# Kernel tuning notes

Hardware: AMD Instinct MI355X
Metric: run time of the kernel (lower is better)

Reference implementation:

```python
import jax, jax.numpy as jnp
import numpy as np

B, N, D, H = 16, 64, 512, 8
DK = D // H


def mish(x):
    return x * jnp.tanh(jax.nn.softplus(x))


def setup_inputs() -> dict:
    key = jax.random.key(0)
    ks = jax.random.split(key, 16)
    s = 1.0 / np.sqrt(D)
    inp = {
        "query_node": jax.random.normal(ks[0], (B, N, D), jnp.float32),
        "value_node": jax.random.normal(ks[1], (B, N, D), jnp.float32),
        "key_edge": jax.random.normal(ks[2], (B, N, N, D), jnp.float32),
        "adj_matrix": jax.random.uniform(ks[3], (B, N, N), jnp.float32),
        "Wq": jax.random.normal(ks[4], (D, D), jnp.float32) * s,
        "bq": jnp.zeros((D,), jnp.float32),
        "Wk": jax.random.normal(ks[5], (D, D), jnp.float32) * s,
        "bk": jnp.zeros((D,), jnp.float32),
        "Wv": jax.random.normal(ks[6], (D, D), jnp.float32) * s,
        "bv": jnp.zeros((D,), jnp.float32),
        "Wn": jax.random.normal(ks[7], (D, D), jnp.float32) * s,
        "bn": jnp.zeros((D,), jnp.float32),
        "We": jax.random.normal(ks[8], (D, D), jnp.float32) * s,
        "be": jnp.zeros((D,), jnp.float32),
    }
    return inp


def reference(query_node, value_node, key_edge, adj_matrix,
              Wq, bq, Wk, bk, Wv, bv, Wn, bn, We, be):
    # distance kernel (computed as in the original; result is unused by attention)
    _adj = jax.nn.softmax(-adj_matrix, axis=-1)

    # projections; heads laid out as in torch .view + transpose/permute
    q = (query_node @ Wq + bq).reshape(B, N, H, DK).transpose(0, 2, 1, 3)          # bhmd
    k = (key_edge @ Wk + bk).reshape(B, N, N, H, DK).transpose(0, 3, 1, 2, 4)      # bhmnd
    v = (value_node @ Wv + bv).reshape(B, N, H, DK).transpose(0, 2, 1, 3)          # bhnd

    inv_sqrt = 1.0 / np.sqrt(DK)
    out_scores = jnp.einsum('bhmd,bhmnd->bhmn', q, k) * inv_sqrt
    in_scores = jnp.einsum('bhnd,bhmnd->bhnm', q, k) * inv_sqrt
    out_attn = jax.nn.softmax(out_scores, axis=-1)
    in_attn = jax.nn.softmax(in_scores, axis=-1)

    # subtract the diagonal of out_attn (counted twice in out+in)
    diag = jnp.einsum('bhnn->bhn', out_attn)
    eye = jnp.eye(N, dtype=out_attn.dtype)
    message = out_attn + in_attn - diag[..., None] * eye  # bhmn (dropout in eval mode = identity)

    node_hidden = jnp.einsum('bhmn,bhnd->bhmd', message, v)
    edge_hidden = message[..., None] * k                   # bhmnd

    node_hidden = node_hidden.transpose(0, 2, 1, 3).reshape(B, N, D)
    edge_hidden = edge_hidden.transpose(0, 2, 3, 1, 4).reshape(B, N, N, D)

    node_out = mish(node_hidden @ Wn + bn)
    edge_out = mish(edge_hidden @ We + be)
    return node_out, edge_out
```

## Files before the change

kernel.cpp:

```cpp
#include <hip/hip_runtime.h>

#define DEV __device__ __forceinline__

typedef __attribute__((ext_vector_type(8))) short short8;
typedef __bf16 bf16x8 __attribute__((ext_vector_type(8)));
typedef __attribute__((ext_vector_type(4))) float f32x4;

constexpr int NB = 16;
constexpr int NN = 64;
constexpr int ND = 512;
constexpr int NH = 8;

DEV float b2f(unsigned short h) { return __uint_as_float(((unsigned)h) << 16); }
DEV unsigned short f2b(float f) {
    unsigned u = __float_as_uint(f);
    return (unsigned short)((u + 0x7fffu + ((u >> 16) & 1u)) >> 16);
}
DEV float mish_fast(float x) {
    float t = __expf(x);
    float w = t * (t + 2.0f);
    float r = x * w * __builtin_amdgcn_rcpf(w + 2.0f);
    return (x > 15.0f) ? x : r;
}
DEV void gload16(const unsigned short* g, unsigned short* lds) {
    __builtin_amdgcn_global_load_lds((const __attribute__((address_space(1))) void*)g,
                                     (__attribute__((address_space(3))) void*)lds,
                                     16, 0, 0);
}

__global__ __launch_bounds__(64)
void probe_dtype(const unsigned* __restrict__ adj, int* __restrict__ flag)
{
    int t = threadIdx.x;
    int c = 0;
#pragma unroll
    for (int i = 0; i < 4; ++i) c += (int)((adj[t * 4 + i] >> 15) & 1u);
    for (int off = 32; off; off >>= 1) c += __shfl_xor(c, off);
    if (t == 0) flag[0] = (c > 32) ? 1 : 0;
}

__global__ __launch_bounds__(256)
void wtrans2(const void* W0, const void* W1, const void* W2, const void* W3,
             const void* W4, unsigned short* __restrict__ out,
             const int* __restrict__ flag)
{
    const void* W = (blockIdx.z == 0) ? W0 : (blockIdx.z == 1) ? W1 :
                    (blockIdx.z == 2) ? W2 : (blockIdx.z == 3) ? W3 : W4;
    const int f32 = flag[0];
    unsigned short* o = out + (size_t)blockIdx.z * 262144;
    __shared__ unsigned short tile[64][65];
    const int t = threadIdx.x;
    const int k0 = blockIdx.x * 64, c0 = blockIdx.y * 64;
#pragma unroll
    for (int rep = 0; rep < 16; ++rep) {
        int idx = rep * 256 + t;
        int r = idx >> 6, c = idx & 63;
        size_t gi = (size_t)(k0 + r) * 512 + c0 + c;
        float v = f32 ? ((const float*)W)[gi]
                      : b2f(((const unsigned short*)W)[gi]);
        tile[r][c] = f2b(v);
    }
    __syncthreads();
#pragma unroll
    for (int rep = 0; rep < 16; ++rep) {
        int idx = rep * 256 + t;
        int cc = idx >> 6, kk = idx & 63;
        int k = k0 + kk;
        o[(size_t)(k >> 5) * 16384 + (size_t)(c0 + cc) * 32 + (k & 31)] = tile[kk][cc];
    }
}

template<int AMODE, bool MISH, bool OUTF32>
__global__ __launch_bounds__(512, 4)
void gemm10(const void* A, long long apitch,
            const unsigned short* __restrict__ Bt2,
            const void* __restrict__ bias_raw,
            const float* __restrict__ msg,
            void* out, long long opitch,
            const int* __restrict__ flag,
            const void* A2, const unsigned short* Bt2b,
            const void* bias2, void* out2)
{
    __shared__ alignas(16) unsigned short As[64][512];
    const int f32g = flag[0];
    const int t = threadIdx.x;
    const int lane = t & 63;
    const int wv = t >> 6;

    long long row0;
    const void* Ap = A; const unsigned short* Btp = Bt2;
    const void* biasp = bias_raw; void* outp = out;
    if (A2 != nullptr && (int)blockIdx.x >= (int)(gridDim.x >> 1)) {
        Ap = A2; Btp = Bt2b; biasp = bias2; outp = out2;
        row0 = (long long)(blockIdx.x - (gridDim.x >> 1)) * 64;
    } else {
        row0 = (long long)blockIdx.x * 64;
    }

    {
        const int r = t >> 3;
        const int q = t & 7;
        const long long gr = row0 + r;
        const float* mrow = nullptr;
        if (AMODE == 2) {
            int b = (int)(gr >> 12), m = (int)(gr >> 6) & 63, n = (int)gr & 63;
            mrow = msg + (((long long)b * 8) * 64 + m) * 64 + n;
        }
        if (AMODE == 0 && f32g) {
            const float* Af = (const float*)Ap + gr * apitch;
#pragma unroll
            for (int i = 0; i < 8; ++i) {
                int g = q + 8 * i;
                f32x4 x0 = *reinterpret_cast<const f32x4*>(Af + g * 8);
                f32x4 x1 = *reinterpret_cast<const f32x4*>(Af + g * 8 + 4);
                short8 sv;
#pragma unroll
                for (int j = 0; j < 4; ++j) {
                    sv[j]     = (short)f2b(x0[j]);
                    sv[j + 4] = (short)f2b(x1[j]);
                }
                *reinterpret_cast<short8*>(&As[r][(g ^ (r & 7)) * 8]) = sv;
            }
        } else {
            const unsigned short* Ah = (const unsigned short*)Ap + gr * apitch;
#pragma unroll
            for (int i = 0; i < 8; ++i) {
                int g = q + 8 * i;
                short8 v = *reinterpret_cast<const short8*>(Ah + g * 8);
                if (AMODE == 2) {
                    float sc = mrow[i * 4096];
#pragma unroll
                    for (int j = 0; j < 8; ++j)
                        v[j] = (short)f2b(b2f((unsigned short)v[j]) * sc);
                }
                *reinterpret_cast<short8*>(&As[r][(g ^ (r & 7)) * 8]) = v;
            }
        }
    }
    __syncthreads();

    const int rA = lane & 15;
    const int p  = lane >> 4;
    const unsigned short* bbase = Btp + ((size_t)(wv * 64 + rA) * 32 + p * 8);

    f32x4 acc[4][4];
#pragma unroll
    for (int mi = 0; mi < 4; ++mi)
#pragma unroll
        for (int ni = 0; ni < 4; ++ni) acc[mi][ni] = f32x4{0.f, 0.f, 0.f, 0.f};

#pragma unroll
    for (int s = 0; s < 16; ++s) {
        bf16x8 bf[4], af[4];
#pragma unroll
        for (int ni = 0; ni < 4; ++ni)
            bf[ni] = *reinterpret_cast<const bf16x8*>(bbase + (size_t)s * 16384 + ni * 512);
#pragma unroll
        for (int mi = 0; mi < 4; ++mi)
            af[mi] = *reinterpret_cast<const bf16x8*>(
                &As[mi * 16 + rA][((((s << 2) | p)) ^ (rA & 7)) << 3]);
#pragma unroll
        for (int mi = 0; mi < 4; ++mi)
#pragma unroll
            for (int ni = 0; ni < 4; ++ni)
                acc[mi][ni] = __builtin_amdgcn_mfma_f32_16x16x32_bf16(
                    af[mi], bf[ni], acc[mi][ni], 0, 0, 0);
    }

    const int orow_q = (lane >> 4) * 4;
#pragma unroll
    for (int mi = 0; mi < 4; ++mi) {
#pragma unroll
        for (int ni = 0; ni < 4; ++ni) {
            int col = wv * 64 + ni * 16 + rA;
            float bz = f32g ? ((const float*)biasp)[col]
                            : b2f(((const unsigned short*)biasp)[col]);
            long long rbase = row0 + mi * 16 + orow_q;
#pragma unroll
            for (int rr = 0; rr < 4; ++rr) {
                float v = acc[mi][ni][rr] + bz;
                if (MISH) v = mish_fast(v);
                long long oi = (rbase + rr) * opitch + col;
                if (OUTF32) ((float*)outp)[oi] = v;
                else        ((unsigned short*)outp)[oi] = f2b(v);
            }
        }
    }
}

__global__ __launch_bounds__(256)
void score_kernel(const unsigned short* __restrict__ q,
                  const unsigned short* __restrict__ kp,
                  float* __restrict__ outS,
                  float* __restrict__ inS)
{
    const int bid = blockIdx.x;
    const int b  = bid >> 5;
    const int i0 = ((bid >> 2) & 7) * 8;
    const int j0 = (bid & 3) * 16;
    const int t = threadIdx.x, lane = t & 63, wv = t >> 6;

    __shared__ alignas(16) unsigned short qs[24][512];
    __shared__ float souts[8][16][8];
    __shared__ float sins[16][8][8];

#pragma unroll
    for (int r8 = 0; r8 < 6; ++r8) {
        int r = wv * 6 + r8;
        int grow = (r < 8) ? (i0 + r) : (j0 + r - 8);
        gload16(q + ((long long)(b * 64 + grow)) * 512 + lane * 8, &qs[r][0]);
    }
    __syncthreads();

    for (int batch = 0; batch < 4; ++batch) {
        const int rbase = wv * 32 + batch * 8;
        short8 kv[8];
#pragma unroll
        for (int u = 0; u < 8; ++u) {
            int r = rbase + u;
            int ii = r >> 4, jj = r & 15;
            kv[u] = *reinterpret_cast<const short8*>(
                kp + ((long long)((b * 64 + i0 + ii) * 64) + j0 + jj) * 1024 + lane * 8);
        }
#pragma unroll
        for (int u = 0; u < 8; ++u) {
            int r = rbase + u;
            int ii = r >> 4, jj = r & 15;
            short8 qi = *reinterpret_cast<const short8*>(&qs[ii][lane * 8]);
            short8 qj = *reinterpret_cast<const short8*>(&qs[8 + jj][lane * 8]);
            float so = 0.f, si = 0.f;
#pragma unroll
            for (int e = 0; e < 8; ++e) {
                float kf = b2f((unsigned short)kv[u][e]);
                so += kf * b2f((unsigned short)qi[e]);
                si += kf * b2f((unsigned short)qj[e]);
            }
#pragma unroll
            for (int off = 1; off < 8; off <<= 1) {
                so += __shfl_xor(so, off);
                si += __shfl_xor(si, off);
            }
            if ((lane & 7) == 0) {
                souts[ii][jj][lane >> 3] = so * 0.125f;
                sins[jj][ii][lane >> 3]  = si * 0.125f;
            }
        }
    }
    __syncthreads();

    {
        int h  = t >> 5;
        int ii = (t >> 2) & 7;
        int qq = t & 3;
        f32x4 v;
#pragma unroll
        for (int e = 0; e < 4; ++e) v[e] = souts[ii][qq * 4 + e][h];
        *reinterpret_cast<f32x4*>(
            &outS[(((long long)(b * 8 + h) * 64) + i0 + ii) * 64 + j0 + qq * 4]) = v;
    }
    {
        int h  = t >> 5;
        int jj = (t >> 1) & 15;
        int hf = t & 1;
        f32x4 v;
#pragma unroll
        for (int e = 0; e < 4; ++e) v[e] = sins[jj][hf * 4 + e][h];
        *reinterpret_cast<f32x4*>(
            &inS[(((long long)(b * 8 + h) * 64) + j0 + jj) * 64 + i0 + hf * 4]) = v;
    }
}

__global__ __launch_bounds__(256)
void softmax_combine(float* __restrict__ outS, const float* __restrict__ inS)
{
    const long long row = (long long)blockIdx.x * 4 + (threadIdx.x >> 6);
    const int l = threadIdx.x & 63;
    const int x = (int)(row & 63);
    float so = outS[row * 64 + l];
    float si = inS[row * 64 + l];
    float mo = so, mi = si;
    for (int off = 32; off; off >>= 1) {
        mo = fmaxf(mo, __shfl_xor(mo, off));
        mi = fmaxf(mi, __shfl_xor(mi, off));
    }
    float eo = __expf(so - mo), ei = __expf(si - mi);
    float zo = eo, zi = ei;
    for (int off = 32; off; off >>= 1) {
        zo += __shfl_xor(zo, off);
        zi += __shfl_xor(zi, off);
    }
    float ao = eo / zo, ai = ei / zi;
    outS[row * 64 + l] = (l == x) ? ai : (ao + ai);
}

__global__ __launch_bounds__(512)
void nh_kernel(const float* __restrict__ msg,
               const unsigned short* __restrict__ v,
               unsigned short* __restrict__ nh)
{
    const int bm = blockIdx.x;
    const int b = bm >> 6, m = bm & 63;
    const int t = threadIdx.x;
    __shared__ float ms2[8 * 64];
    ms2[t] = msg[((long long)b * 8 + (t >> 6)) * 4096 + m * 64 + (t & 63)];
    __syncthreads();
    const float* mrow = &ms2[(t >> 6) * 64];
    float acc = 0.f;
#pragma unroll 8
    for (int n = 0; n < 64; ++n)
        acc += mrow[n] * b2f(v[((long long)b * 64 + n) * 512 + t]);
    nh[(long long)bm * 1024 + t] = f2b(acc);
}

extern "C" void kernel_launch(void* const* d_in, const int* in_sizes, int n_in,
                              void* d_out, int out_size, void* d_ws, size_t ws_size,
                              hipStream_t stream)
{
    const void* qn = d_in[0];
    const void* vn = d_in[1];
    const void* ke = d_in[2];
    const unsigned* adj = (const unsigned*)d_in[3];
    const void* Wq = d_in[4];  const void* bq = d_in[5];
    const void* Wk = d_in[6];  const void* bk = d_in[7];
    const void* Wv = d_in[8];  const void* bv = d_in[9];
    const void* Wn = d_in[10]; const void* bn = d_in[11];
    const void* We = d_in[12]; const void* be = d_in[13];

    float* out_node = (float*)d_out;
    float* out_edge = out_node + (size_t)NB * NN * ND;
    unsigned short* kp = (unsigned short*)out_edge;
    unsigned short* nh = (unsigned short*)out_node;
    float* inS = out_node;

    char* wsb = (char*)d_ws;
    int* flag = (int*)wsb;
    unsigned short* Wt  = (unsigned short*)(wsb + 16);
    unsigned short* Wqt = Wt + 0 * 262144;
    unsigned short* Wkt = Wt + 1 * 262144;
    unsigned short* Wvt = Wt + 2 * 262144;
    unsigned short* Wnt = Wt + 3 * 262144;
    unsigned short* Wet = Wt + 4 * 262144;
    unsigned short* q_ws = Wt + 5 * 262144;
    unsigned short* v_ws = q_ws + 524288;
    float* msg = (float*)(v_ws + 524288);

    probe_dtype<<<1, 64, 0, stream>>>(adj, flag);
    wtrans2<<<dim3(8, 8, 5), 256, 0, stream>>>(Wq, Wk, Wv, Wn, We, Wt, flag);
    gemm10<0, false, false><<<32, 512, 0, stream>>>(
        qn, 512, Wqt, bq, nullptr, q_ws, 512, flag, vn, Wvt, bv, v_ws);
    gemm10<0, false, false><<<1024, 512, 0, stream>>>(
        ke, 512, Wkt, bk, nullptr, kp, 1024, flag, nullptr, nullptr, nullptr, nullptr);
    score_kernel<<<512, 256, 0, stream>>>(q_ws, kp, msg, inS);
    softmax_combine<<<2048, 256, 0, stream>>>(msg, inS);
    nh_kernel<<<NB * NN, 512, 0, stream>>>(msg, v_ws, nh);
    gemm10<1, true, true><<<16, 512, 0, stream>>>(
        nh, 1024, Wnt, bn, nullptr, out_node, 512, flag, nullptr, nullptr, nullptr, nullptr);
    gemm10<2, true, true><<<1024, 512, 0, stream>>>(
        kp, 1024, Wet, be, msg, out_edge, 512, flag, nullptr, nullptr, nullptr, nullptr);
}
```

Before: 198.4 us.

## Halve GEMM block to 256 threads with 128-column warp tiles and staged bf16 stores

The GEMM kernel now runs 4 waves per block instead of 8, and each wave computes 64x128 outputs (32 MFMA accumulators) rather than 64x64. This doubles B-fragment reuse per A-fragment load. The XOR swizzle on the LDS A tile is replaced by row padding (520 columns). For bf16 outputs, results are first staged through LDS so the global writes become coalesced 16-byte rows. The cost is higher register pressure (128 accumulator VGPRs per lane) and fewer waves per block to hide global B loads.

Result: slower. 217.6 us (+9.7%).

```diff
diff --git a/kernel.cpp b/kernel.cpp
--- a/kernel.cpp
+++ b/kernel.cpp
@@ -71,8 +71,8 @@
 }
 
 template<int AMODE, bool MISH, bool OUTF32>
-__global__ __launch_bounds__(512, 4)
-void gemm10(const void* A, long long apitch,
+__global__ __launch_bounds__(256, 2)
+void gemm11(const void* A, long long apitch,
             const unsigned short* __restrict__ Bt2,
             const void* __restrict__ bias_raw,
             const float* __restrict__ msg,
@@ -81,7 +81,7 @@
             const void* A2, const unsigned short* Bt2b,
             const void* bias2, void* out2)
 {
-    __shared__ alignas(16) unsigned short As[64][512];
+    __shared__ alignas(16) unsigned short As[64][520];
     const int f32g = flag[0];
     const int t = threadIdx.x;
     const int lane = t & 63;
@@ -98,8 +98,8 @@
     }
 
     {
-        const int r = t >> 3;
-        const int q = t & 7;
+        const int r = t >> 2;
+        const int q = t & 3;
         const long long gr = row0 + r;
         const float* mrow = nullptr;
         if (AMODE == 2) {
@@ -109,8 +109,8 @@
         if (AMODE == 0 && f32g) {
             const float* Af = (const float*)Ap + gr * apitch;
 #pragma unroll
-            for (int i = 0; i < 8; ++i) {
-                int g = q + 8 * i;
+            for (int i = 0; i < 16; ++i) {
+                int g = q + 4 * i;
                 f32x4 x0 = *reinterpret_cast<const f32x4*>(Af + g * 8);
                 f32x4 x1 = *reinterpret_cast<const f32x4*>(Af + g * 8 + 4);
                 short8 sv;
@@ -119,21 +119,21 @@
                     sv[j]     = (short)f2b(x0[j]);
                     sv[j + 4] = (short)f2b(x1[j]);
                 }
-                *reinterpret_cast<short8*>(&As[r][(g ^ (r & 7)) * 8]) = sv;
+                *reinterpret_cast<short8*>(&As[r][g * 8]) = sv;
             }
         } else {
             const unsigned short* Ah = (const unsigned short*)Ap + gr * apitch;
 #pragma unroll
-            for (int i = 0; i < 8; ++i) {
-                int g = q + 8 * i;
+            for (int i = 0; i < 16; ++i) {
+                int g = q + 4 * i;
                 short8 v = *reinterpret_cast<const short8*>(Ah + g * 8);
                 if (AMODE == 2) {
-                    float sc = mrow[i * 4096];
+                    float sc = mrow[(g >> 3) * 4096];
 #pragma unroll
                     for (int j = 0; j < 8; ++j)
                         v[j] = (short)f2b(b2f((unsigned short)v[j]) * sc);
                 }
-                *reinterpret_cast<short8*>(&As[r][(g ^ (r & 7)) * 8]) = v;
+                *reinterpret_cast<short8*>(&As[r][g * 8]) = v;
             }
         }
     }
@@ -141,49 +141,77 @@
 
     const int rA = lane & 15;
     const int p  = lane >> 4;
-    const unsigned short* bbase = Btp + ((size_t)(wv * 64 + rA) * 32 + p * 8);
-
-    f32x4 acc[4][4];
+    const unsigned short* bbase = Btp + ((size_t)(wv * 128 + rA) * 32 + p * 8);
+
+    f32x4 acc[4][8];
 #pragma unroll
     for (int mi = 0; mi < 4; ++mi)
 #pragma unroll
-        for (int ni = 0; ni < 4; ++ni) acc[mi][ni] = f32x4{0.f, 0.f, 0.f, 0.f};
+        for (int ni = 0; ni < 8; ++ni) acc[mi][ni] = f32x4{0.f, 0.f, 0.f, 0.f};
 
 #pragma unroll
     for (int s = 0; s < 16; ++s) {
-        bf16x8 bf[4], af[4];
-#pragma unroll
-        for (int ni = 0; ni < 4; ++ni)
+        bf16x8 bf[8], af[4];
+#pragma unroll
+        for (int ni = 0; ni < 8; ++ni)
             bf[ni] = *reinterpret_cast<const bf16x8*>(bbase + (size_t)s * 16384 + ni * 512);
 #pragma unroll
         for (int mi = 0; mi < 4; ++mi)
             af[mi] = *reinterpret_cast<const bf16x8*>(
-                &As[mi * 16 + rA][((((s << 2) | p)) ^ (rA & 7)) << 3]);
+                &As[mi * 16 + rA][(s * 4 + p) * 8]);
 #pragma unroll
         for (int mi = 0; mi < 4; ++mi)
 #pragma unroll
-            for (int ni = 0; ni < 4; ++ni)
+            for (int ni = 0; ni < 8; ++ni)
                 acc[mi][ni] = __builtin_amdgcn_mfma_f32_16x16x32_bf16(
                     af[mi], bf[ni], acc[mi][ni], 0, 0, 0);
     }
 
     const int orow_q = (lane >> 4) * 4;
-#pragma unroll
-    for (int mi = 0; mi < 4; ++mi) {
-#pragma unroll
-        for (int ni = 0; ni < 4; ++ni) {
-            int col = wv * 64 + ni * 16 + rA;
-            float bz = f32g ? ((const float*)biasp)[col]
-                            : b2f(((const unsigned short*)biasp)[col]);
-            long long rbase = row0 + mi * 16 + orow_q;
-#pragma unroll
-            for (int rr = 0; rr < 4; ++rr) {
-                float v = acc[mi][ni][rr] + bz;
-                if (MISH) v = mish_fast(v);
-                long long oi = (rbase + rr) * opitch + col;
-                if (OUTF32) ((float*)outp)[oi] = v;
-                else        ((unsigned short*)outp)[oi] = f2b(v);
-            }
+    if (OUTF32) {
+#pragma unroll
+        for (int mi = 0; mi < 4; ++mi) {
+#pragma unroll
+            for (int ni = 0; ni < 8; ++ni) {
+                int col = wv * 128 + ni * 16 + rA;
+                float bz = f32g ? ((const float*)biasp)[col]
+                                : b2f(((const unsigned short*)biasp)[col]);
+                long long rbase = row0 + mi * 16 + orow_q;
+#pragma unroll
+                for (int rr = 0; rr < 4; ++rr) {
+                    float v = acc[mi][ni][rr] + bz;
+                    if (MISH) v = mish_fast(v);
+                    ((float*)outp)[(rbase + rr) * opitch + col] = v;
+                }
+            }
+        }
+    } else {
+        __syncthreads();
+#pragma unroll
+        for (int mi = 0; mi < 4; ++mi) {
+#pragma unroll
+            for (int ni = 0; ni < 8; ++ni) {
+                int col = wv * 128 + ni * 16 + rA;
+                float bz = f32g ? ((const float*)biasp)[col]
+                                : b2f(((const unsigned short*)biasp)[col]);
+                int rbase = mi * 16 + orow_q;
+#pragma unroll
+                for (int rr = 0; rr < 4; ++rr) {
+                    float v = acc[mi][ni][rr] + bz;
+                    if (MISH) v = mish_fast(v);
+                    As[rbase + rr][col] = f2b(v);
+                }
+            }
+        }
+        __syncthreads();
+        const int r = t >> 2;
+        const int q = t & 3;
+        unsigned short* orow = (unsigned short*)outp + (row0 + r) * opitch;
+#pragma unroll
+        for (int i = 0; i < 16; ++i) {
+            int g = q + 4 * i;
+            *reinterpret_cast<short8*>(orow + g * 8) =
+                *reinterpret_cast<const short8*>(&As[r][g * 8]);
         }
     }
 }
@@ -346,15 +374,15 @@
 
     probe_dtype<<<1, 64, 0, stream>>>(adj, flag);
     wtrans2<<<dim3(8, 8, 5), 256, 0, stream>>>(Wq, Wk, Wv, Wn, We, Wt, flag);
-    gemm10<0, false, false><<<32, 512, 0, stream>>>(
+    gemm11<0, false, false><<<32, 256, 0, stream>>>(
         qn, 512, Wqt, bq, nullptr, q_ws, 512, flag, vn, Wvt, bv, v_ws);
-    gemm10<0, false, false><<<1024, 512, 0, stream>>>(
+    gemm11<0, false, false><<<1024, 256, 0, stream>>>(
         ke, 512, Wkt, bk, nullptr, kp, 1024, flag, nullptr, nullptr, nullptr, nullptr);
     score_kernel<<<512, 256, 0, stream>>>(q_ws, kp, msg, inS);
     softmax_combine<<<2048, 256, 0, stream>>>(msg, inS);
     nh_kernel<<<NB * NN, 512, 0, stream>>>(msg, v_ws, nh);
-    gemm10<1, true, true><<<16, 512, 0, stream>>>(
+    gemm11<1, true, true><<<16, 256, 0, stream>>>(
         nh, 1024, Wnt, bn, nullptr, out_node, 512, flag, nullptr, nullptr, nullptr, nullptr);
-    gemm10<2, true, true><<<1024, 512, 0, stream>>>(
+    gemm11<2, true, true><<<1024, 256, 0, stream>>>(
         kp, 1024, Wet, be, msg, out_edge, 512, flag, nullptr, nullptr, nullptr, nullptr);
 }
```

## Make GEMMs persistent with double-buffered 32-row panels and merged launches

Applied to the files above, without the earlier changes.

Replaces the one-shot 64-row GEMM kernel with a persistent kernel that walks 32-row panels in a grid-stride loop. The next panel's global loads are issued before the current panel's MFMA loop and written into a second LDS buffer, so loading overlaps compute. The Q/V/K projections now share one launch, and so do the node and edge output GEMMs, which removes launches and fills the machine more evenly. Each panel does half the MFMA work per B-fragment load, so weight traffic from L2 per output row rises. The extra registers held for prefetch may lower occupancy.

New measurement: 245.2 us. +23.6%, slower.

```diff
diff --git a/kernel.cpp b/kernel.cpp
--- a/kernel.cpp
+++ b/kernel.cpp
@@ -70,121 +70,173 @@
     }
 }
 
-template<int AMODE, bool MISH, bool OUTF32>
+struct GSrc {
+    const void* A;
+    const unsigned short* Bt;
+    const void* bias;
+    void* out;
+    long long apitch;
+    long long opitch;
+    int npanels;
+};
+
+template<bool PROJ>
 __global__ __launch_bounds__(512, 4)
-void gemm10(const void* A, long long apitch,
-            const unsigned short* __restrict__ Bt2,
-            const void* __restrict__ bias_raw,
+void gemm12(GSrc s0, GSrc s1, GSrc s2,
             const float* __restrict__ msg,
-            void* out, long long opitch,
-            const int* __restrict__ flag,
-            const void* A2, const unsigned short* Bt2b,
-            const void* bias2, void* out2)
-{
-    __shared__ alignas(16) unsigned short As[64][512];
+            const int* __restrict__ flag, int nblocks)
+{
+    __shared__ alignas(16) unsigned short As[2][32][512];
     const int f32g = flag[0];
+    const int totp = s0.npanels + s1.npanels + s2.npanels;
     const int t = threadIdx.x;
     const int lane = t & 63;
     const int wv = t >> 6;
-
-    long long row0;
-    const void* Ap = A; const unsigned short* Btp = Bt2;
-    const void* biasp = bias_raw; void* outp = out;
-    if (A2 != nullptr && (int)blockIdx.x >= (int)(gridDim.x >> 1)) {
-        Ap = A2; Btp = Bt2b; biasp = bias2; outp = out2;
-        row0 = (long long)(blockIdx.x - (gridDim.x >> 1)) * 64;
-    } else {
-        row0 = (long long)blockIdx.x * 64;
-    }
-
-    {
-        const int r = t >> 3;
-        const int q = t & 7;
-        const long long gr = row0 + r;
-        const float* mrow = nullptr;
-        if (AMODE == 2) {
-            int b = (int)(gr >> 12), m = (int)(gr >> 6) & 63, n = (int)gr & 63;
-            mrow = msg + (((long long)b * 8) * 64 + m) * 64 + n;
-        }
-        if (AMODE == 0 && f32g) {
-            const float* Af = (const float*)Ap + gr * apitch;
-#pragma unroll
-            for (int i = 0; i < 8; ++i) {
-                int g = q + 8 * i;
-                f32x4 x0 = *reinterpret_cast<const f32x4*>(Af + g * 8);
-                f32x4 x1 = *reinterpret_cast<const f32x4*>(Af + g * 8 + 4);
-                short8 sv;
-#pragma unroll
-                for (int j = 0; j < 4; ++j) {
-                    sv[j]     = (short)f2b(x0[j]);
-                    sv[j + 4] = (short)f2b(x1[j]);
-                }
-                *reinterpret_cast<short8*>(&As[r][(g ^ (r & 7)) * 8]) = sv;
-            }
-        } else {
-            const unsigned short* Ah = (const unsigned short*)Ap + gr * apitch;
-#pragma unroll
-            for (int i = 0; i < 8; ++i) {
-                int g = q + 8 * i;
-                short8 v = *reinterpret_cast<const short8*>(Ah + g * 8);
-                if (AMODE == 2) {
-                    float sc = mrow[i * 4096];
-#pragma unroll
-                    for (int j = 0; j < 8; ++j)
-                        v[j] = (short)f2b(b2f((unsigned short)v[j]) * sc);
-                }
-                *reinterpret_cast<short8*>(&As[r][(g ^ (r & 7)) * 8]) = v;
-            }
-        }
-    }
-    __syncthreads();
-
     const int rA = lane & 15;
     const int p  = lane >> 4;
-    const unsigned short* bbase = Btp + ((size_t)(wv * 64 + rA) * 32 + p * 8);
-
-    f32x4 acc[4][4];
-#pragma unroll
-    for (int mi = 0; mi < 4; ++mi)
-#pragma unroll
-        for (int ni = 0; ni < 4; ++ni) acc[mi][ni] = f32x4{0.f, 0.f, 0.f, 0.f};
-
-#pragma unroll
-    for (int s = 0; s < 16; ++s) {
-        bf16x8 bf[4], af[4];
-#pragma unroll
-        for (int ni = 0; ni < 4; ++ni)
-            bf[ni] = *reinterpret_cast<const bf16x8*>(bbase + (size_t)s * 16384 + ni * 512);
-#pragma unroll
-        for (int mi = 0; mi < 4; ++mi)
-            af[mi] = *reinterpret_cast<const bf16x8*>(
-                &As[mi * 16 + rA][((((s << 2) | p)) ^ (rA & 7)) << 3]);
-#pragma unroll
-        for (int mi = 0; mi < 4; ++mi)
+    const int sr = t >> 4;
+    const int sq = t & 15;
+
+    int pc = blockIdx.x;
+    if (pc >= totp) return;
+
+    GSrc gc, gn;
+    long long rc = 0, rn = 0;
+    bool uc = false, un = false;
+
+    auto selectSrc = [&](int pp, GSrc& g, long long& prow, bool& umsg) {
+        if (pp < s0.npanels) { g = s0; prow = (long long)pp * 32; umsg = !PROJ; }
+        else if (pp < s0.npanels + s1.npanels) {
+            g = s1; prow = (long long)(pp - s0.npanels) * 32; umsg = false;
+        } else {
+            g = s2; prow = (long long)(pp - s0.npanels - s1.npanels) * 32; umsg = false;
+        }
+    };
+
+    f32x4 pf[8];
+    short8 ph[4];
+    float pscale = 1.0f;
+
+    auto loadPanel = [&](const GSrc& g, long long prow, bool umsg) {
+        long long gr = prow + sr;
+        if (PROJ && f32g) {
+            const float* src = (const float*)g.A + gr * g.apitch + sq * 32;
+#pragma unroll
+            for (int i = 0; i < 8; ++i)
+                pf[i] = *reinterpret_cast<const f32x4*>(src + i * 4);
+        } else {
+            const unsigned short* src = (const unsigned short*)g.A + gr * g.apitch + sq * 32;
+#pragma unroll
+            for (int i = 0; i < 4; ++i)
+                ph[i] = *reinterpret_cast<const short8*>(src + i * 8);
+            if (!PROJ) {
+                if (umsg) {
+                    int b = (int)(gr >> 12), m = (int)(gr >> 6) & 63, n = (int)gr & 63;
+                    pscale = msg[(((long long)b * 8 + (sq >> 1)) << 12) + m * 64 + n];
+                } else {
+                    pscale = 1.0f;
+                }
+            }
+        }
+    };
+
+    auto writePanel = [&](int buf) {
+        short8 sv[4];
+        if (PROJ && f32g) {
+#pragma unroll
+            for (int i = 0; i < 4; ++i) {
+#pragma unroll
+                for (int j = 0; j < 4; ++j) {
+                    sv[i][j]     = (short)f2b(pf[2 * i][j]);
+                    sv[i][j + 4] = (short)f2b(pf[2 * i + 1][j]);
+                }
+            }
+        } else {
+#pragma unroll
+            for (int i = 0; i < 4; ++i) {
+                sv[i] = ph[i];
+                if (!PROJ) {
+#pragma unroll
+                    for (int j = 0; j < 8; ++j)
+                        sv[i][j] = (short)f2b(b2f((unsigned short)sv[i][j]) * pscale);
+                }
+            }
+        }
+#pragma unroll
+        for (int i = 0; i < 4; ++i) {
+            int g = sq * 4 + i;
+            *reinterpret_cast<short8*>(&As[buf][sr][(g ^ (sr & 7)) * 8]) = sv[i];
+        }
+    };
+
+    selectSrc(pc, gc, rc, uc);
+    loadPanel(gc, rc, uc);
+    writePanel(0);
+    __syncthreads();
+    int cur = 0;
+
+    for (;;) {
+        const int pn = pc + nblocks;
+        const bool have_next = pn < totp;
+        if (have_next) { selectSrc(pn, gn, rn, un); loadPanel(gn, rn, un); }
+
+        f32x4 acc[2][4];
+#pragma unroll
+        for (int mi = 0; mi < 2; ++mi)
+#pragma unroll
+            for (int ni = 0; ni < 4; ++ni) acc[mi][ni] = f32x4{0.f, 0.f, 0.f, 0.f};
+
+        const unsigned short* bbase = gc.Bt + ((size_t)(wv * 64 + rA) * 32 + p * 8);
+#pragma unroll
+        for (int s = 0; s < 16; ++s) {
+            bf16x8 bf[4], af[2];
 #pragma unroll
             for (int ni = 0; ni < 4; ++ni)
-                acc[mi][ni] = __builtin_amdgcn_mfma_f32_16x16x32_bf16(
-                    af[mi], bf[ni], acc[mi][ni], 0, 0, 0);
-    }
-
-    const int orow_q = (lane >> 4) * 4;
-#pragma unroll
-    for (int mi = 0; mi < 4; ++mi) {
-#pragma unroll
-        for (int ni = 0; ni < 4; ++ni) {
-            int col = wv * 64 + ni * 16 + rA;
-            float bz = f32g ? ((const float*)biasp)[col]
-                            : b2f(((const unsigned short*)biasp)[col]);
-            long long rbase = row0 + mi * 16 + orow_q;
-#pragma unroll
-            for (int rr = 0; rr < 4; ++rr) {
-                float v = acc[mi][ni][rr] + bz;
-                if (MISH) v = mish_fast(v);
-                long long oi = (rbase + rr) * opitch + col;
-                if (OUTF32) ((float*)outp)[oi] = v;
-                else        ((unsigned short*)outp)[oi] = f2b(v);
-            }
-        }
+                bf[ni] = *reinterpret_cast<const bf16x8*>(
+                    bbase + (size_t)s * 16384 + ni * 512);
+#pragma unroll
+            for (int mi = 0; mi < 2; ++mi) {
+                int r = mi * 16 + rA;
+                af[mi] = *reinterpret_cast<const bf16x8*>(
+                    &As[cur][r][((s * 4 + p) ^ (r & 7)) * 8]);
+            }
+#pragma unroll
+            for (int mi = 0; mi < 2; ++mi)
+#pragma unroll
+                for (int ni = 0; ni < 4; ++ni)
+                    acc[mi][ni] = __builtin_amdgcn_mfma_f32_16x16x32_bf16(
+                        af[mi], bf[ni], acc[mi][ni], 0, 0, 0);
+        }
+
+        if (have_next) {
+            writePanel(cur ^ 1);
+            __syncthreads();
+        }
+
+        {
+            const int orow_q = (lane >> 4) * 4;
+#pragma unroll
+            for (int mi = 0; mi < 2; ++mi) {
+#pragma unroll
+                for (int ni = 0; ni < 4; ++ni) {
+                    int col = wv * 64 + ni * 16 + rA;
+                    float bz = f32g ? ((const float*)gc.bias)[col]
+                                    : b2f(((const unsigned short*)gc.bias)[col]);
+                    long long rbase = rc + mi * 16 + orow_q;
+#pragma unroll
+                    for (int rr = 0; rr < 4; ++rr) {
+                        float v = acc[mi][ni][rr] + bz;
+                        if (!PROJ) v = mish_fast(v);
+                        long long oi = (rbase + rr) * gc.opitch + col;
+                        if (!PROJ) ((float*)gc.out)[oi] = v;
+                        else       ((unsigned short*)gc.out)[oi] = f2b(v);
+                    }
+                }
+            }
+        }
+
+        if (!have_next) break;
+        pc = pn; gc = gn; rc = rn; uc = un; cur ^= 1;
     }
 }
 
@@ -346,15 +398,20 @@
 
     probe_dtype<<<1, 64, 0, stream>>>(adj, flag);
     wtrans2<<<dim3(8, 8, 5), 256, 0, stream>>>(Wq, Wk, Wv, Wn, We, Wt, flag);
-    gemm10<0, false, false><<<32, 512, 0, stream>>>(
-        qn, 512, Wqt, bq, nullptr, q_ws, 512, flag, vn, Wvt, bv, v_ws);
-    gemm10<0, false, false><<<1024, 512, 0, stream>>>(
-        ke, 512, Wkt, bk, nullptr, kp, 1024, flag, nullptr, nullptr, nullptr, nullptr);
+
+    {
+        GSrc sk{ke, Wkt, bk, kp,   512, 1024, 2048};
+        GSrc sq{qn, Wqt, bq, q_ws, 512,  512,   32};
+        GSrc sv{vn, Wvt, bv, v_ws, 512,  512,   32};
+        gemm12<true><<<512, 512, 0, stream>>>(sk, sq, sv, nullptr, flag, 512);
+    }
     score_kernel<<<512, 256, 0, stream>>>(q_ws, kp, msg, inS);
     softmax_combine<<<2048, 256, 0, stream>>>(msg, inS);
     nh_kernel<<<NB * NN, 512, 0, stream>>>(msg, v_ws, nh);
-    gemm10<1, true, true><<<16, 512, 0, stream>>>(
-        nh, 1024, Wnt, bn, nullptr, out_node, 512, flag, nullptr, nullptr, nullptr, nullptr);
-    gemm10<2, true, true><<<1024, 512, 0, stream>>>(
-        kp, 1024, Wet, be, msg, out_edge, 512, flag, nullptr, nullptr, nullptr, nullptr);
-}
+    {
+        GSrc se{kp, Wet, be, out_edge, 1024, 512, 2048};
+        GSrc sn{nh, Wnt, bn, out_node, 1024, 512,   32};
+        GSrc sz{nullptr, nullptr, nullptr, nullptr, 0, 0, 0};
+        gemm12<false><<<512, 512, 0, stream>>>(se, sn, sz, msg, flag, 512);
+    }
+}
```
